# Kernel tuning notes

Hardware: AMD Instinct MI355X
Metric: run time of the kernel (lower is better)

## Reference

```python
import math
import jax, jax.numpy as jnp
import numpy as np

B, C, M = 32, 1024, 1024
D, DV, R_ANCHOR = 512, 512, 64


def setup_inputs() -> dict:
    key = jax.random.key(0)
    ks = jax.random.split(key, 6)
    return {
        "T": jax.random.normal(ks[0], (B, C, M), dtype=jnp.float32),
        "Wq": jax.random.normal(ks[1], (C, D), dtype=jnp.float32) * 0.02,
        "Wk": jax.random.normal(ks[2], (C, D), dtype=jnp.float32) * 0.02,
        "Wv": jax.random.normal(ks[3], (C, DV), dtype=jnp.float32) * 0.02,
        "Wout": jax.random.normal(ks[4], (DV, C), dtype=jnp.float32) * 0.02,
        "R_full": jax.random.normal(ks[5], (R_ANCHOR, M), dtype=jnp.float32) * 0.02,
    }


def reference(T, Wq, Wk, Wv, Wout, R_full):
    # T: [B, C, m] -> tokens-major [B, m, C]
    b, c, m = T.shape
    T_mC = jnp.swapaxes(T, 1, 2)
    Q = T_mC @ Wq           # [B, m, D]
    K = T_mC @ Wk           # [B, m, D]
    V = T_mC @ Wv           # [B, m, DV]
    Rm = R_full[:, :m]      # [r, m]
    # Faithful to original torch einsum: m and j are summed INDEPENDENTLY
    # (outer product of row-sums of R with token-sums of K/V), not contracted.
    K_proj = jnp.einsum('rm,bjd->brd', Rm, K)   # [B, r, D]
    V_proj = jnp.einsum('rm,bjd->brd', Rm, V)   # [B, r, DV]
    scale = 1.0 / math.sqrt(max(1.0, float(Wq.shape[1])))
    scores = jnp.einsum('bid,btd->bit', Q, K_proj) * scale  # [B, m, r]
    A = jax.nn.softmax(scores, axis=-1)
    T_out_mdv = jnp.einsum('bir,brd->bid', A, V_proj)       # [B, m, DV]
    T_out_C = T_out_mdv @ Wout                               # [B, m, C]
    return jnp.swapaxes(T_out_C, 1, 2)                       # [B, C, m]
```

## Files before the change

kernel.cpp:

```cpp
#include <hip/hip_runtime.h>
#include <math.h>

constexpr int Bc  = 32;
constexpr int Cc  = 1024;
constexpr int Mc  = 1024;
constexpr int Dc  = 512;
constexpr int DVc = 512;
constexpr int Rc  = 64;

typedef float f4 __attribute__((ext_vector_type(4)));

__global__ __launch_bounds__(256) void k_kv1(const float* __restrict__ T,
                                             const float* __restrict__ Wk,
                                             const float* __restrict__ Wv,
                                             float* __restrict__ pK,
                                             float* __restrict__ pV) {
    __shared__ float ts[64];
    const int cs  = blockIdx.x;
    const int b   = blockIdx.y;
    const int c0  = cs * 64;
    const int tid = threadIdx.x;
    const int w   = tid >> 6, lane = tid & 63;

    const float* Tb = T + ((long)b * Cc + c0) * Mc;
#pragma unroll 4
    for (int r = w * 16; r < w * 16 + 16; ++r) {
        const float* row = Tb + (long)r * Mc;
        float s = 0.f;
#pragma unroll
        for (int k = 0; k < 4; ++k) {
            float4 t = *(const float4*)&row[k * 256 + lane * 4];
            s += (t.x + t.y) + (t.z + t.w);
        }
#pragma unroll
        for (int off = 32; off; off >>= 1) s += __shfl_down(s, off, 64);
        if (lane == 0) ts[r] = s;
    }
    __syncthreads();

    const int d = tid;
    float k1 = 0.f, k2 = 0.f, v1 = 0.f, v2 = 0.f;
#pragma unroll 4
    for (int c = 0; c < 64; ++c) {
        float t = ts[c];
        const float* wkr = Wk + (long)(c0 + c) * Dc;
        const float* wvr = Wv + (long)(c0 + c) * DVc;
        k1 = fmaf(t, wkr[d],       k1);
        k2 = fmaf(t, wkr[d + 256], k2);
        v1 = fmaf(t, wvr[d],       v1);
        v2 = fmaf(t, wvr[d + 256], v2);
    }
    const long base = ((long)b * 16 + cs) * 512;
    pK[base + d] = k1;  pK[base + d + 256] = k2;
    pV[base + d] = v1;  pV[base + d + 256] = v2;
}

__global__ __launch_bounds__(256) void k_kv2r(const float* __restrict__ pK,
                                              const float* __restrict__ pV,
                                              float* __restrict__ Ksum,
                                              float* __restrict__ Vsum,
                                              const float* __restrict__ Rfull,
                                              float* __restrict__ rsum) {
    if (blockIdx.x < 128) {
        const int gid = blockIdx.x * 256 + threadIdx.x;
        const int sel = gid >> 14;
        const int rem = gid & 16383;
        const float* p = (sel ? pV : pK) + (long)(rem >> 9) * 16 * 512 + (rem & 511);
        float s = 0.f;
#pragma unroll
        for (int i = 0; i < 16; ++i) s += p[i * 512];
        (sel ? Vsum : Ksum)[rem] = s;
    } else {
        const int row  = (blockIdx.x - 128) * 4 + (threadIdx.x >> 6);
        const int lane = threadIdx.x & 63;
        const float* xr = Rfull + (long)row * 1024;
        float s = 0.f;
#pragma unroll
        for (int k = 0; k < 4; ++k) {
            float4 t = *(const float4*)&xr[k * 256 + lane * 4];
            s += (t.x + t.y) + (t.z + t.w);
        }
#pragma unroll
        for (int off = 32; off; off >>= 1) s += __shfl_down(s, off, 64);
        if (lane == 0) rsum[row] = s;
    }
}

__global__ __launch_bounds__(256) void k_mid(const float* __restrict__ Wq,
                                             const float* __restrict__ Ksum,
                                             float* __restrict__ wqk,
                                             const float* __restrict__ Wout,
                                             const float* __restrict__ Vsum,
                                             float* __restrict__ pVW) {
    __shared__ float vs[64];
    if (blockIdx.x < 8192) {
        const int wid  = blockIdx.x * 4 + (threadIdx.x >> 6);
        const int lane = threadIdx.x & 63;
        const float* wq = Wq + (long)(wid & 1023) * Dc;
        const float* ks = Ksum + (wid >> 10) * Dc;
        float s = 0.f;
#pragma unroll
        for (int k = 0; k < 4; ++k) {
            int d = k * 128 + lane * 2;
            float2 a = *(const float2*)&wq[d];
            float2 x = *(const float2*)&ks[d];
            s = fmaf(a.x, x.x, s);
            s = fmaf(a.y, x.y, s);
        }
#pragma unroll
        for (int off = 32; off; off >>= 1) s += __shfl_down(s, off, 64);
        if (lane == 0) wqk[wid] = s;
    } else {
        const int idx = blockIdx.x - 8192;
        const int ds  = idx & 7;
        const int b   = idx >> 3;
        const int d0  = ds * 64;
        const int tid = threadIdx.x;
        if (tid < 64) vs[tid] = Vsum[b * Dc + d0 + tid];
        __syncthreads();
        float a0 = 0.f, a1 = 0.f, a2 = 0.f, a3 = 0.f;
        const float* W0 = Wout + (long)d0 * Cc + tid;
#pragma unroll 4
        for (int d = 0; d < 64; ++d) {
            float v = vs[d];
            const float* wr = W0 + (long)d * Cc;
            a0 = fmaf(v, wr[0],   a0);
            a1 = fmaf(v, wr[256], a1);
            a2 = fmaf(v, wr[512], a2);
            a3 = fmaf(v, wr[768], a3);
        }
        const long base = ((long)b * 8 + ds) * 1024 + tid;
        pVW[base] = a0;  pVW[base + 256] = a1;
        pVW[base + 512] = a2;  pVW[base + 768] = a3;
    }
}

__global__ __launch_bounds__(256) void k_vw2(const float* __restrict__ pVW,
                                             float* __restrict__ vw) {
    const int gid = blockIdx.x * 256 + threadIdx.x;
    const float* p = pVW + (long)(gid >> 10) * 8 * 1024 + (gid & 1023);
    float s = 0.f;
#pragma unroll
    for (int i = 0; i < 8; ++i) s += p[i * 1024];
    vw[gid] = s;
}

__global__ __launch_bounds__(256) void k_final(const float* __restrict__ T,
                                               const float* __restrict__ wqk,
                                               const float* __restrict__ vw,
                                               const float* __restrict__ rsum,
                                               float* __restrict__ Out,
                                               float scale) {
    __shared__ float rs[64];
    __shared__ float part[16][72];
    __shared__ float wsh[64];
    __shared__ float wql[Cc];
    __shared__ float vwl[Cc];

    const int b  = blockIdx.y;
    const int m0 = blockIdx.x * 64;
    const int il = threadIdx.x & 15;
    const int cs = threadIdx.x >> 4;

    ((float4*)wql)[threadIdx.x] = ((const float4*)(wqk + b * Cc))[threadIdx.x];
    ((float4*)vwl)[threadIdx.x] = ((const float4*)(vw + b * Cc))[threadIdx.x];
    if (threadIdx.x < 64) rs[threadIdx.x] = rsum[threadIdx.x];
    __syncthreads();

    const float* Tbm = T + (long)b * Cc * Mc + m0 + il * 4;

    float4 acc = make_float4(0.f, 0.f, 0.f, 0.f);
#pragma unroll 8
    for (int c = cs; c < Cc; c += 16) {
        float4 t = *(const float4*)&Tbm[(long)c * Mc];
        float wc = wql[c];
        acc.x = fmaf(t.x, wc, acc.x);
        acc.y = fmaf(t.y, wc, acc.y);
        acc.z = fmaf(t.z, wc, acc.z);
        acc.w = fmaf(t.w, wc, acc.w);
    }
    *(float4*)&part[cs][il * 4] = acc;
    __syncthreads();

    if (threadIdx.x < 64) {
        const int i = threadIdx.x;
        float q = 0.f;
#pragma unroll
        for (int k = 0; k < 16; ++k) q += part[k][i];
        q *= scale;
        float mx = -1e30f;
#pragma unroll
        for (int r = 0; r < 64; ++r) mx = fmaxf(mx, q * rs[r]);
        float se = 0.f, sw = 0.f;
#pragma unroll
        for (int r = 0; r < 64; ++r) {
            float e = __expf(q * rs[r] - mx);
            se += e;
            sw = fmaf(e, rs[r], sw);
        }
        wsh[i] = sw / se;
    }
    __syncthreads();

    float* Ob = Out + (long)b * Cc * Mc + m0 + il * 4;
    float4 w4 = *(const float4*)&wsh[il * 4];
#pragma unroll 4
    for (int c = cs; c < Cc; c += 16) {
        float v = vwl[c];
        f4 o = {w4.x * v, w4.y * v, w4.z * v, w4.w * v};
        __builtin_nontemporal_store(o, (f4*)&Ob[(long)c * Mc]);
    }
}

extern "C" void kernel_launch(void* const* d_in, const int* in_sizes, int n_in,
                              void* d_out, int out_size, void* d_ws, size_t ws_size,
                              hipStream_t stream) {
    const float* T     = (const float*)d_in[0];
    const float* Wq    = (const float*)d_in[1];
    const float* Wk    = (const float*)d_in[2];
    const float* Wv    = (const float*)d_in[3];
    const float* Wout  = (const float*)d_in[4];
    const float* Rfull = (const float*)d_in[5];
    float* Out = (float*)d_out;

    float* ws   = (float*)d_ws;
    float* rsum = ws;
    float* Ksum = rsum + Rc;
    float* Vsum = Ksum + Bc * Dc;
    float* wqk  = Vsum + Bc * DVc;
    float* vw   = wqk + Bc * Cc;
    float* pK   = vw + Bc * Cc;
    float* pV   = pK + 262144;
    float* pVW  = pV + 262144;

    k_kv1<<<dim3(16, Bc), 256, 0, stream>>>(T, Wk, Wv, pK, pV);
    k_kv2r<<<144, 256, 0, stream>>>(pK, pV, Ksum, Vsum, Rfull, rsum);
    k_mid<<<8448, 256, 0, stream>>>(Wq, Ksum, wqk, Wout, Vsum, pVW);
    k_vw2<<<128, 256, 0, stream>>>(pVW, vw);
    const float scale = 1.0f / sqrtf((float)Dc);
    k_final<<<dim3(Mc / 64, Bc), 256, 0, stream>>>(T, wqk, vw, rsum, Out, scale);
}
```

Measured before the change: 295.2 us.

## Fold vw reduction into final kernel and double block size to 512

```diff
diff --git a/kernel.cpp b/kernel.cpp
--- a/kernel.cpp
+++ b/kernel.cpp
@@ -10,7 +10,7 @@
 
 typedef float f4 __attribute__((ext_vector_type(4)));
 
-__global__ __launch_bounds__(256) void k_kv1(const float* __restrict__ T,
+__global__ __launch_bounds__(512) void k_kv1(const float* __restrict__ T,
                                              const float* __restrict__ Wk,
                                              const float* __restrict__ Wv,
                                              float* __restrict__ pK,
@@ -24,7 +24,7 @@
 
     const float* Tb = T + ((long)b * Cc + c0) * Mc;
 #pragma unroll 4
-    for (int r = w * 16; r < w * 16 + 16; ++r) {
+    for (int r = w * 8; r < w * 8 + 8; ++r) {
         const float* row = Tb + (long)r * Mc;
         float s = 0.f;
 #pragma unroll
@@ -39,20 +39,16 @@
     __syncthreads();
 
     const int d = tid;
-    float k1 = 0.f, k2 = 0.f, v1 = 0.f, v2 = 0.f;
+    float k1 = 0.f, v1 = 0.f;
 #pragma unroll 4
     for (int c = 0; c < 64; ++c) {
         float t = ts[c];
-        const float* wkr = Wk + (long)(c0 + c) * Dc;
-        const float* wvr = Wv + (long)(c0 + c) * DVc;
-        k1 = fmaf(t, wkr[d],       k1);
-        k2 = fmaf(t, wkr[d + 256], k2);
-        v1 = fmaf(t, wvr[d],       v1);
-        v2 = fmaf(t, wvr[d + 256], v2);
+        k1 = fmaf(t, Wk[(long)(c0 + c) * Dc  + d], k1);
+        v1 = fmaf(t, Wv[(long)(c0 + c) * DVc + d], v1);
     }
     const long base = ((long)b * 16 + cs) * 512;
-    pK[base + d] = k1;  pK[base + d + 256] = k2;
-    pV[base + d] = v1;  pV[base + d + 256] = v2;
+    pK[base + d] = k1;
+    pV[base + d] = v1;
 }
 
 __global__ __launch_bounds__(256) void k_kv2r(const float* __restrict__ pK,
@@ -135,43 +131,41 @@
     }
 }
 
-__global__ __launch_bounds__(256) void k_vw2(const float* __restrict__ pVW,
-                                             float* __restrict__ vw) {
-    const int gid = blockIdx.x * 256 + threadIdx.x;
-    const float* p = pVW + (long)(gid >> 10) * 8 * 1024 + (gid & 1023);
-    float s = 0.f;
-#pragma unroll
-    for (int i = 0; i < 8; ++i) s += p[i * 1024];
-    vw[gid] = s;
-}
-
-__global__ __launch_bounds__(256) void k_final(const float* __restrict__ T,
+__global__ __launch_bounds__(512) void k_final(const float* __restrict__ T,
                                                const float* __restrict__ wqk,
-                                               const float* __restrict__ vw,
+                                               const float* __restrict__ pVW,
                                                const float* __restrict__ rsum,
                                                float* __restrict__ Out,
                                                float scale) {
     __shared__ float rs[64];
-    __shared__ float part[16][72];
+    __shared__ float part[32][72];
     __shared__ float wsh[64];
     __shared__ float wql[Cc];
     __shared__ float vwl[Cc];
 
-    const int b  = blockIdx.y;
-    const int m0 = blockIdx.x * 64;
-    const int il = threadIdx.x & 15;
-    const int cs = threadIdx.x >> 4;
-
-    ((float4*)wql)[threadIdx.x] = ((const float4*)(wqk + b * Cc))[threadIdx.x];
-    ((float4*)vwl)[threadIdx.x] = ((const float4*)(vw + b * Cc))[threadIdx.x];
-    if (threadIdx.x < 64) rs[threadIdx.x] = rsum[threadIdx.x];
+    const int b   = blockIdx.y;
+    const int m0  = blockIdx.x * 64;
+    const int tid = threadIdx.x;
+    const int il  = tid & 15;
+    const int cs  = tid >> 4;
+
+    if (tid < 256) ((float4*)wql)[tid] = ((const float4*)(wqk + b * Cc))[tid];
+#pragma unroll
+    for (int c = tid; c < Cc; c += 512) {
+        const float* p = pVW + (long)b * 8 * 1024 + c;
+        float s = 0.f;
+#pragma unroll
+        for (int j = 0; j < 8; ++j) s += p[j * 1024];
+        vwl[c] = s;
+    }
+    if (tid < 64) rs[tid] = rsum[tid];
     __syncthreads();
 
     const float* Tbm = T + (long)b * Cc * Mc + m0 + il * 4;
 
     float4 acc = make_float4(0.f, 0.f, 0.f, 0.f);
 #pragma unroll 8
-    for (int c = cs; c < Cc; c += 16) {
+    for (int c = cs; c < Cc; c += 32) {
         float4 t = *(const float4*)&Tbm[(long)c * Mc];
         float wc = wql[c];
         acc.x = fmaf(t.x, wc, acc.x);
@@ -182,11 +176,11 @@
     *(float4*)&part[cs][il * 4] = acc;
     __syncthreads();
 
-    if (threadIdx.x < 64) {
-        const int i = threadIdx.x;
+    if (tid < 64) {
+        const int i = tid;
         float q = 0.f;
 #pragma unroll
-        for (int k = 0; k < 16; ++k) q += part[k][i];
+        for (int k = 0; k < 32; ++k) q += part[k][i];
         q *= scale;
         float mx = -1e30f;
 #pragma unroll
@@ -205,7 +199,7 @@
     float* Ob = Out + (long)b * Cc * Mc + m0 + il * 4;
     float4 w4 = *(const float4*)&wsh[il * 4];
 #pragma unroll 4
-    for (int c = cs; c < Cc; c += 16) {
+    for (int c = cs; c < Cc; c += 32) {
         float v = vwl[c];
         f4 o = {w4.x * v, w4.y * v, w4.z * v, w4.w * v};
         __builtin_nontemporal_store(o, (f4*)&Ob[(long)c * Mc]);
@@ -233,10 +227,9 @@
     float* pV   = pK + 262144;
     float* pVW  = pV + 262144;
 
-    k_kv1<<<dim3(16, Bc), 256, 0, stream>>>(T, Wk, Wv, pK, pV);
+    k_kv1<<<dim3(16, Bc), 512, 0, stream>>>(T, Wk, Wv, pK, pV);
     k_kv2r<<<144, 256, 0, stream>>>(pK, pV, Ksum, Vsum, Rfull, rsum);
     k_mid<<<8448, 256, 0, stream>>>(Wq, Ksum, wqk, Wout, Vsum, pVW);
-    k_vw2<<<128, 256, 0, stream>>>(pVW, vw);
     const float scale = 1.0f / sqrtf((float)Dc);
-    k_final<<<dim3(Mc / 64, Bc), 256, 0, stream>>>(T, wqk, vw, rsum, Out, scale);
-}
+    k_final<<<dim3(Mc / 64, Bc), 512, 0, stream>>>(T, wqk, pVW, rsum, Out, scale);
+}
```

New measurement: 290.4 us. Within noise of the previous version (-1.6%).
